# Kernel tuning notes

Hardware: AMD Instinct MI355X
Metric: run time of the kernel (lower is better)

The kernel has to match this reference:

```python
import jax, jax.numpy as jnp
import numpy as np

B, S, HID = 2, 2048, 2048
H, KV, D, E = 16, 4, 128, 32
NB = 9  # num_behavior + 1
EPS = 1e-6
SCALING = (E + D) ** -0.5


def rmsnorm(x, w, eps=EPS):
    # normalize over last dim in fp32, like Qwen3MoeRMSNorm
    xf = x.astype(jnp.float32)
    var = jnp.mean(xf * xf, axis=-1, keepdims=True)
    return (xf * jax.lax.rsqrt(var + eps)).astype(x.dtype) * w


def setup_inputs() -> dict:
    key = jax.random.key(0)
    ks = jax.random.split(key, 12)
    s = lambda n: 1.0 / np.sqrt(n)
    return {
        "hidden_states": jax.random.normal(ks[0], (B, S, HID), jnp.float32),
        "behavior_index": jax.random.randint(ks[1], (B, S), 0, NB),
        "q_proj_w": jax.random.normal(ks[2], (H * D, HID), jnp.float32) * s(HID),
        "k_proj_w": jax.random.normal(ks[3], (KV * D, HID), jnp.float32) * s(HID),
        "v_proj_w": jax.random.normal(ks[4], (KV * D, HID), jnp.float32) * s(HID),
        "o_proj_w": jax.random.normal(ks[5], (HID, H * D), jnp.float32) * s(H * D),
        "q_norm_w": jnp.ones((D,), jnp.float32),
        "k_norm_w": jnp.ones((D,), jnp.float32),
        "qbe_table": jax.random.normal(ks[6], (NB, H * E), jnp.float32),
        "kbe_table": jax.random.normal(ks[7], (NB, KV * E), jnp.float32),
        "qbn_w": jnp.ones((E,), jnp.float32),
        "kbn_w": jnp.ones((E,), jnp.float32),
    }


def reference(hidden_states, behavior_index, q_proj_w, k_proj_w, v_proj_w,
              o_proj_w, q_norm_w, k_norm_w, qbe_table, kbe_table, qbn_w, kbn_w):
    b, s, _ = hidden_states.shape
    # QKV projections + per-head RMSNorm on q/k
    q = rmsnorm((hidden_states @ q_proj_w.T).reshape(b, s, H, D), q_norm_w)
    k = rmsnorm((hidden_states @ k_proj_w.T).reshape(b, s, KV, D), k_norm_w)
    v = (hidden_states @ v_proj_w.T).reshape(b, s, KV, D)
    q = q.transpose(0, 2, 1, 3)  # [b,H,s,D]
    k = k.transpose(0, 2, 1, 3)  # [b,KV,s,D]
    v = v.transpose(0, 2, 1, 3)  # [b,KV,s,D]
    # behavior embeddings: lookup -> per-head RMSNorm -> concat onto head_dim
    qbe = rmsnorm(qbe_table[behavior_index].reshape(b, s, H, E), qbn_w).transpose(0, 2, 1, 3)
    kbe = rmsnorm(kbe_table[behavior_index].reshape(b, s, KV, E), kbn_w).transpose(0, 2, 1, 3)
    q = jnp.concatenate([q, qbe], axis=-1)  # [b,H,s,D+E]
    k = jnp.concatenate([k, kbe], axis=-1)  # [b,KV,s,D+E]
    # GQA: repeat kv heads
    g = H // KV
    k = jnp.repeat(k, g, axis=1)
    v = jnp.repeat(v, g, axis=1)
    # eager attention, causal, softmax in fp32
    scores = jnp.einsum('bhqd,bhkd->bhqk', q, k) * SCALING
    causal = jnp.tril(jnp.ones((s, s), bool))
    scores = jnp.where(causal, scores, jnp.finfo(scores.dtype).min)
    attn = jax.nn.softmax(scores.astype(jnp.float32), axis=-1).astype(q.dtype)
    out = jnp.einsum('bhqk,bhkd->bhqd', attn, v)  # [b,H,s,D]
    out = out.transpose(0, 2, 1, 3).reshape(b, s, H * D)
    return out @ o_proj_w.T
```

## Files before the change

kernel.cpp:

```cpp
#include <hip/hip_runtime.h>

typedef unsigned short u16;
typedef unsigned int u32;
typedef __bf16 bf16x8 __attribute__((ext_vector_type(8)));
typedef __bf16 b16x4 __attribute__((ext_vector_type(4)));
typedef short s16x4 __attribute__((ext_vector_type(4)));
typedef float f32x4 __attribute__((ext_vector_type(4)));

#define SCALE 0.07905694150420949f
#define LOG2E 1.4426950408889634f

__device__ __forceinline__ float bf2f(u16 h) { return __uint_as_float(((u32)h) << 16); }
__device__ __forceinline__ u16 f2bf(float f) {
  u32 u = __float_as_uint(f);
  u += 0x7fffu + ((u >> 16) & 1u);
  return (u16)(u >> 16);
}
__device__ __forceinline__ u16 f2bf_fast(float f) {
  return (u16)((__float_as_uint(f) + 0x8000u) >> 16);
}
__device__ __forceinline__ bf16x8 ldfrag(const u16* p) {
  int4 t = *reinterpret_cast<const int4*>(p);
  return __builtin_bit_cast(bf16x8, t);
}

__device__ __forceinline__ f32x4 mfma16x16(s16x4 a, s16x4 b, f32x4 c) {
#if __has_builtin(__builtin_amdgcn_mfma_f32_16x16x16bf16_1k)
  return __builtin_amdgcn_mfma_f32_16x16x16bf16_1k(a, b, c, 0, 0, 0);
#elif __has_builtin(__builtin_amdgcn_mfma_f32_16x16x16_bf16)
  return __builtin_amdgcn_mfma_f32_16x16x16_bf16(__builtin_bit_cast(b16x4, a),
                                                 __builtin_bit_cast(b16x4, b), c, 0, 0, 0);
#else
  asm volatile("s_nop 2\n\tv_mfma_f32_16x16x16_bf16 %0, %1, %2, %0"
               : "+v"(c) : "v"(a), "v"(b));
  return c;
#endif
}

__device__ __forceinline__ void gld16(const u16* g, u16* l) {
  __builtin_amdgcn_global_load_lds((const __attribute__((address_space(1))) u32*)(const void*)g,
                                   (__attribute__((address_space(3))) u32*)(void*)l, 16, 0, 0);
}

__global__ void conv_all(const float* __restrict__ hs, const float* __restrict__ qw,
                         const float* __restrict__ kw, const float* __restrict__ vw,
                         const float* __restrict__ ow, u16* __restrict__ hs_bf,
                         u16* __restrict__ wqkv, u16* __restrict__ ow_bf) {
  const int total = 4718592;
  for (int i = blockIdx.x * blockDim.x + threadIdx.x; i < total; i += gridDim.x * blockDim.x) {
    const float* src;
    u16* dst;
    int j = i;
    if (j < 2097152) {
      src = hs; dst = hs_bf;
    } else if (j < 3145728) {
      j -= 2097152; src = qw; dst = wqkv;
    } else if (j < 3407872) {
      j -= 3145728; src = kw; dst = wqkv + 4194304;
    } else if (j < 3670016) {
      j -= 3407872; src = vw; dst = wqkv + 5242880;
    } else {
      j -= 3670016; src = ow; dst = ow_bf;
    }
    float4 v = reinterpret_cast<const float4*>(src)[j];
    ushort4 o = {f2bf(v.x), f2bf(v.y), f2bf(v.z), f2bf(v.w)};
    reinterpret_cast<ushort4*>(dst)[j] = o;
  }
}

template <int OUT_BF16>
__global__ __launch_bounds__(256, 2) void gemm_bt(const u16* __restrict__ A,
                                                  const u16* __restrict__ Bw,
                                                  void* __restrict__ Cv,
                                                  int M, int N, int K) {
  __shared__ __align__(16) u16 As[2][8192];
  __shared__ __align__(16) u16 Bs[2][8192];
  const int tid = threadIdx.x;
  const int nbn = N >> 7;
  const int cpx = gridDim.x >> 3;
  const int swz = (blockIdx.x & 7) * cpx + (blockIdx.x >> 3);
  const int bm = swz / nbn, bn = swz % nbn;
  const int row0 = bm << 7, col0 = bn << 7;
  const int lane = tid & 63, w = tid >> 6;
  const int lg = lane >> 4, lr = lane & 15;
  const int wr = w >> 1, wc = w & 1;
  const int nt = K >> 6;

  auto stage = [&](int slot, int t) {
    const size_t k0 = (size_t)t << 6;
#pragma unroll
    for (int it = 0; it < 4; ++it) {
      int G = it * 256 + tid;
      int r = G >> 3, p = G & 7;
      int gs = p ^ (r & 7);
      gld16(&A[(size_t)(row0 + r) * K + k0 + gs * 8], &As[slot][(size_t)G * 8]);
      gld16(&Bw[(size_t)(col0 + r) * K + k0 + gs * 8], &Bs[slot][(size_t)G * 8]);
    }
  };

  f32x4 acc[4][4] = {};
  stage(0, 0);
  if (nt > 1) stage(1, 1);

  for (int t = 0; t < nt; ++t) {
    const int slot = t & 1;
    if (t + 1 < nt) {
      asm volatile("s_waitcnt vmcnt(8)" ::: "memory");
    } else {
      asm volatile("s_waitcnt vmcnt(0)" ::: "memory");
    }
    __builtin_amdgcn_s_barrier();
    __builtin_amdgcn_sched_barrier(0);
#pragma unroll
    for (int kk = 0; kk < 2; ++kk) {
      bf16x8 af[4], bv[4];
#pragma unroll
      for (int m = 0; m < 4; ++m) {
        int r = wr * 64 + m * 16 + lr;
        int g = (kk * 4 + lg) ^ (lr & 7);
        af[m] = ldfrag(&As[slot][r * 64 + g * 8]);
      }
#pragma unroll
      for (int n = 0; n < 4; ++n) {
        int r = wc * 64 + n * 16 + lr;
        int g = (kk * 4 + lg) ^ (lr & 7);
        bv[n] = ldfrag(&Bs[slot][r * 64 + g * 8]);
      }
#pragma unroll
      for (int m = 0; m < 4; ++m)
#pragma unroll
        for (int n = 0; n < 4; ++n)
          acc[m][n] = __builtin_amdgcn_mfma_f32_16x16x32_bf16(af[m], bv[n], acc[m][n], 0, 0, 0);
    }
    __builtin_amdgcn_sched_barrier(0);
    __builtin_amdgcn_s_barrier();
    if (t + 2 < nt) stage(slot, t + 2);
  }

#pragma unroll
  for (int m = 0; m < 4; ++m)
#pragma unroll
    for (int n = 0; n < 4; ++n)
#pragma unroll
      for (int r = 0; r < 4; ++r) {
        int row = row0 + wr * 64 + m * 16 + lg * 4 + r;
        int col = col0 + wc * 64 + n * 16 + lr;
        float v = acc[m][n][r];
        if (OUT_BF16)
          ((u16*)Cv)[(size_t)row * N + col] = f2bf(v);
        else
          ((float*)Cv)[(size_t)row * N + col] = v;
      }
}

__global__ __launch_bounds__(256) void postproc(
    const u16* __restrict__ qkv, const int* __restrict__ bidx,
    const float* __restrict__ qnw, const float* __restrict__ knw,
    const float* __restrict__ qbe_t, const float* __restrict__ kbe_t,
    const float* __restrict__ qbn, const float* __restrict__ kbn,
    u16* __restrict__ qcat, u16* __restrict__ kcat, u16* __restrict__ vt) {
  const int tok = blockIdx.x;
  const int b = tok >> 11, s = tok & 2047;
  const int w = threadIdx.x >> 6, lane = threadIdx.x & 63;
  const int idx = bidx[tok];
  const u16* base = qkv + (size_t)tok * 3072;
  const float QS = SCALE * LOG2E;

  for (int h = w; h < 16; h += 4) {
    float x0 = bf2f(base[h * 128 + 2 * lane]);
    float x1 = bf2f(base[h * 128 + 2 * lane + 1]);
    float ss = x0 * x0 + x1 * x1;
#pragma unroll
    for (int o = 32; o; o >>= 1) ss += __shfl_xor(ss, o);
    float rn = rsqrtf(ss * (1.f / 128.f) + 1e-6f) * QS;
    size_t ob = ((size_t)(b * 16 + h) * 2048 + s) * 160;
    u32 pk = (u32)f2bf(x0 * rn * qnw[2 * lane]) |
             ((u32)f2bf(x1 * rn * qnw[2 * lane + 1]) << 16);
    *reinterpret_cast<u32*>(&qcat[ob + 2 * lane]) = pk;
    if (lane < 32) {
      float e = qbe_t[idx * 512 + h * 32 + lane];
      float s2 = e * e;
#pragma unroll
      for (int o = 16; o; o >>= 1) s2 += __shfl_xor(s2, o);
      qcat[ob + 128 + lane] = f2bf(e * rsqrtf(s2 * (1.f / 32.f) + 1e-6f) * qbn[lane] * QS);
    }
  }
  {
    const int kv = w;
    float x0 = bf2f(base[2048 + kv * 128 + 2 * lane]);
    float x1 = bf2f(base[2048 + kv * 128 + 2 * lane + 1]);
    float ss = x0 * x0 + x1 * x1;
#pragma unroll
    for (int o = 32; o; o >>= 1) ss += __shfl_xor(ss, o);
    float rn = rsqrtf(ss * (1.f / 128.f) + 1e-6f);
    size_t ob = ((size_t)(b * 4 + kv) * 2048 + s) * 160;
    u32 pk = (u32)f2bf(x0 * rn * knw[2 * lane]) |
             ((u32)f2bf(x1 * rn * knw[2 * lane + 1]) << 16);
    *reinterpret_cast<u32*>(&kcat[ob + 2 * lane]) = pk;
    if (lane < 32) {
      float e = kbe_t[idx * 128 + kv * 32 + lane];
      float s2 = e * e;
#pragma unroll
      for (int o = 16; o; o >>= 1) s2 += __shfl_xor(s2, o);
      kcat[ob + 128 + lane] = f2bf(e * rsqrtf(s2 * (1.f / 32.f) + 1e-6f) * kbn[lane]);
    }
    size_t vb = (size_t)(b * 4 + kv) * 128 * 2048;
    vt[vb + (size_t)lane * 2048 + s] = base[2560 + kv * 128 + lane];
    vt[vb + (size_t)(lane + 64) * 2048 + s] = base[2560 + kv * 128 + 64 + lane];
  }
}

__global__ __launch_bounds__(256, 2) void attn(const u16* __restrict__ qcat,
                                               const u16* __restrict__ kcat,
                                               const u16* __restrict__ vt,
                                               u16* __restrict__ aout) {
  __shared__ __align__(16) u16 Kls[2][10240];
  __shared__ __align__(16) u16 Vls[8192];
  const int tid = threadIdx.x;
  const int blk = blockIdx.x;
  const int kvh = blk & 3;
  const int b = (blk >> 2) & 1;
  const int hq = (blk >> 3) & 3;
  const int gsel = blk >> 5;
  const int g = (gsel < 8) ? gsel : 23 - gsel;
  const int h = kvh * 4 + hq;
  const int w = tid >> 6;
  const int lane = tid & 63;
  const int lg = lane >> 4, lr = lane & 15;
  const int qb_a = g * 4 + w;
  const int qb_b = 127 - qb_a;
  const int qpa = qb_a * 16 + lr;
  const int qpb = qb_b * 16 + lr;
  const int nt = 32 - g;

  const u16* qpA = qcat + ((size_t)(b * 16 + h) * 2048 + qb_a * 16) * 160;
  const u16* qpB = qcat + ((size_t)(b * 16 + h) * 2048 + qb_b * 16) * 160;
  bf16x8 qfa[5], qfb[5];
#pragma unroll
  for (int c = 0; c < 5; ++c) {
    qfa[c] = ldfrag(qpA + lr * 160 + c * 32 + lg * 8);
    qfb[c] = ldfrag(qpB + lr * 160 + c * 32 + lg * 8);
  }

  const u16* kbp = kcat + (size_t)(b * 4 + kvh) * 2048 * 160;
  const u16* vbp = vt + (size_t)(b * 4 + kvh) * 128 * 2048;

  auto stageK = [&](int buf, int kt) {
    const u16* ksrc = kbp + (size_t)kt * (64 * 160);
#pragma unroll
    for (int it = 0; it < 5; ++it) {
      int G = it * 256 + tid;
      int r = G / 20, p = G - r * 20;
      int gs = p ^ ((r >> 1) & 3);
      gld16(ksrc + r * 160 + gs * 8, &Kls[buf][G * 8]);
    }
  };
  auto stageV = [&](int kt) {
    const u16* vsrc = vbp + kt * 64;
#pragma unroll
    for (int it = 0; it < 4; ++it) {
      int G = it * 256 + tid;
      int r = G >> 3, p = G & 7;
      int gs = p ^ (r & 7);
      gld16(vsrc + (size_t)r * 2048 + gs * 8, &Vls[G * 8]);
    }
  };

  float ma = -INFINITY, la = 0.f, mb = -INFINITY, lb = 0.f;
  f32x4 acc_a[8] = {}, acc_b[8] = {};

  stageK(0, 0);
  stageV(0);
  __syncthreads();

  for (int kt = 0; kt < nt; ++kt) {
    const int buf = kt & 1;
    const bool aact = (kt <= g);
    if (kt + 1 < nt) stageK(buf ^ 1, kt + 1);

    f32x4 sa[4] = {}, sb[4] = {};
#pragma unroll
    for (int c = 0; c < 5; ++c) {
      bf16x8 kf[4];
#pragma unroll
      for (int i = 0; i < 4; ++i) {
        int r = i * 16 + lr;
        int p = (c * 4 + lg) ^ ((r >> 1) & 3);
        kf[i] = ldfrag(&Kls[buf][(r * 20 + p) * 8]);
      }
#pragma unroll
      for (int i = 0; i < 4; ++i)
        sb[i] = __builtin_amdgcn_mfma_f32_16x16x32_bf16(kf[i], qfb[c], sb[i], 0, 0, 0);
      if (aact)
#pragma unroll
        for (int i = 0; i < 4; ++i)
          sa[i] = __builtin_amdgcn_mfma_f32_16x16x32_bf16(kf[i], qfa[c], sa[i], 0, 0, 0);
    }

    s16x4 pka[4], pkb[4];
    auto soft = [&](f32x4 (&st)[4], float& mm, float& ls, f32x4 (&ac)[8], s16x4 (&pk)[4],
                    bool masked, int qpos) {
      float vmax = -INFINITY;
#pragma unroll
      for (int i = 0; i < 4; ++i)
#pragma unroll
        for (int r = 0; r < 4; ++r) {
          float v = st[i][r];
          if (masked && (kt * 64 + i * 16 + 4 * lg + r > qpos)) v = -INFINITY;
          st[i][r] = v;
          vmax = fmaxf(vmax, v);
        }
      vmax = fmaxf(vmax, __shfl_xor(vmax, 16));
      vmax = fmaxf(vmax, __shfl_xor(vmax, 32));
      bool skip = __all(vmax <= mm + 8.f);
      float mn = skip ? mm : fmaxf(mm, vmax);
      float rs = 0.f;
#pragma unroll
      for (int i = 0; i < 4; ++i)
#pragma unroll
        for (int r = 0; r < 4; ++r) {
          float p = exp2f(st[i][r] - mn);
          st[i][r] = p;
          rs += p;
        }
      rs += __shfl_xor(rs, 16);
      rs += __shfl_xor(rs, 32);
      if (skip) {
        ls += rs;
      } else {
        float corr = exp2f(mm - mn);
        ls = ls * corr + rs;
        mm = mn;
        float c4[4];
#pragma unroll
        for (int r = 0; r < 4; ++r) c4[r] = __shfl(corr, 4 * lg + r);
#pragma unroll
        for (int dt = 0; dt < 8; ++dt)
#pragma unroll
          for (int r = 0; r < 4; ++r) ac[dt][r] *= c4[r];
      }
#pragma unroll
      for (int i = 0; i < 4; ++i) {
        pk[i][0] = (short)f2bf_fast(st[i][0]);
        pk[i][1] = (short)f2bf_fast(st[i][1]);
        pk[i][2] = (short)f2bf_fast(st[i][2]);
        pk[i][3] = (short)f2bf_fast(st[i][3]);
      }
    };
    soft(sb, mb, lb, acc_b, pkb, kt == nt - 1, qpb);
    if (aact) soft(sa, ma, la, acc_a, pka, kt == g, qpa);

    __syncthreads();

#pragma unroll
    for (int ks = 0; ks < 4; ++ks) {
      s16x4 vf[8];
#pragma unroll
      for (int dt = 0; dt < 8; ++dt) {
        int r = dt * 16 + lr;
        int p = (ks * 2 + (lg >> 1)) ^ (r & 7);
        vf[dt] = *reinterpret_cast<const s16x4*>(&Vls[(r * 8 + p) * 8 + (lg & 1) * 4]);
      }
#pragma unroll
      for (int dt = 0; dt < 8; ++dt) acc_b[dt] = mfma16x16(pkb[ks], vf[dt], acc_b[dt]);
      if (aact)
#pragma unroll
        for (int dt = 0; dt < 8; ++dt) acc_a[dt] = mfma16x16(pka[ks], vf[dt], acc_a[dt]);
    }

    __syncthreads();
    if (kt + 1 < nt) stageV(kt + 1);
  }

  float inva[4], invb[4];
#pragma unroll
  for (int r = 0; r < 4; ++r) {
    inva[r] = 1.f / __shfl(la, 4 * lg + r);
    invb[r] = 1.f / __shfl(lb, 4 * lg + r);
  }
#pragma unroll
  for (int dt = 0; dt < 8; ++dt)
#pragma unroll
    for (int r = 0; r < 4; ++r) {
      int rowa = qb_a * 16 + 4 * lg + r;
      int rowb = qb_b * 16 + 4 * lg + r;
      aout[((size_t)(b * 2048 + rowa) * 16 + h) * 128 + dt * 16 + lr] =
          f2bf(acc_a[dt][r] * inva[r]);
      aout[((size_t)(b * 2048 + rowb) * 16 + h) * 128 + dt * 16 + lr] =
          f2bf(acc_b[dt][r] * invb[r]);
    }
}

extern "C" void kernel_launch(void* const* d_in, const int* in_sizes, int n_in,
                              void* d_out, int out_size, void* d_ws, size_t ws_size,
                              hipStream_t stream) {
  const float* hs = (const float*)d_in[0];
  const int* bidx = (const int*)d_in[1];
  const float* qw = (const float*)d_in[2];
  const float* kw = (const float*)d_in[3];
  const float* vw = (const float*)d_in[4];
  const float* ow = (const float*)d_in[5];
  const float* qnw = (const float*)d_in[6];
  const float* knw = (const float*)d_in[7];
  const float* qbe_t = (const float*)d_in[8];
  const float* kbe_t = (const float*)d_in[9];
  const float* qbn = (const float*)d_in[10];
  const float* kbn = (const float*)d_in[11];

  u16* ws = (u16*)d_ws;
  u16* hs_bf = ws;
  u16* wqkv = hs_bf + 8388608;
  u16* ow_bf = wqkv + 6291456;
  u16* qkv = ow_bf + 4194304;
  u16* qcat = qkv + 12582912;
  u16* kcat = qcat + 10485760;
  u16* vt = kcat + 2621440;
  u16* attn_o = vt + 2097152;

  conv_all<<<4608, 256, 0, stream>>>(hs, qw, kw, vw, ow, hs_bf, wqkv, ow_bf);

  gemm_bt<1><<<dim3((4096 / 128) * (3072 / 128)), 256, 0, stream>>>(
      hs_bf, wqkv, (void*)qkv, 4096, 3072, 2048);

  postproc<<<4096, 256, 0, stream>>>(qkv, bidx, qnw, knw, qbe_t, kbe_t, qbn, kbn,
                                     qcat, kcat, vt);

  attn<<<512, 256, 0, stream>>>(qcat, kcat, vt, attn_o);

  gemm_bt<0><<<dim3((4096 / 128) * (2048 / 128)), 256, 0, stream>>>(
      attn_o, ow_bf, (void*)d_out, 4096, 2048, 2048);
}
```

Baseline: 223.1 us.

## Fuse QK RMSNorm, behavior-embedding concat and V transpose into QKV GEMM epilogue

Removes the separate postproc kernel by doing the per-head RMSNorm, behavior-embedding lookup and normalization, and V transpose inside the QKV GEMM epilogue. The sum of squares for each head is reduced across the tile with lane shuffles plus a small shared-memory exchange. This avoids writing and re-reading the bf16 qkv intermediate and saves one launch. In exchange the epilogue writes scalar 2-byte values with scattered strides (especially the V transpose) and adds a barrier and per-thread embedding loops.

Measured after the change: 217.6 us. 2.5% less time.

```diff
diff --git a/kernel.cpp b/kernel.cpp
--- a/kernel.cpp
+++ b/kernel.cpp
@@ -68,13 +68,17 @@
   }
 }
 
-template <int OUT_BF16>
-__global__ __launch_bounds__(256, 2) void gemm_bt(const u16* __restrict__ A,
-                                                  const u16* __restrict__ Bw,
-                                                  void* __restrict__ Cv,
-                                                  int M, int N, int K) {
+template <int MODE>
+__global__ __launch_bounds__(256, 2) void gemm_bt(
+    const u16* __restrict__ A, const u16* __restrict__ Bw, void* __restrict__ Cv,
+    int M, int N, int K,
+    const int* __restrict__ bidx, const float* __restrict__ qnw, const float* __restrict__ knw,
+    const float* __restrict__ qbe_t, const float* __restrict__ kbe_t,
+    const float* __restrict__ qbn, const float* __restrict__ kbn,
+    u16* __restrict__ qcat, u16* __restrict__ kcat, u16* __restrict__ vt) {
   __shared__ __align__(16) u16 As[2][8192];
   __shared__ __align__(16) u16 Bs[2][8192];
+  __shared__ float red[128][2];
   const int tid = threadIdx.x;
   const int nbn = N >> 7;
   const int cpx = gridDim.x >> 3;
@@ -137,76 +141,108 @@
     if (t + 2 < nt) stage(slot, t + 2);
   }
 
-#pragma unroll
-  for (int m = 0; m < 4; ++m)
-#pragma unroll
-    for (int n = 0; n < 4; ++n)
+  if (MODE == 0) {
+#pragma unroll
+    for (int m = 0; m < 4; ++m)
+#pragma unroll
+      for (int n = 0; n < 4; ++n)
+#pragma unroll
+        for (int r = 0; r < 4; ++r) {
+          int row = row0 + wr * 64 + m * 16 + lg * 4 + r;
+          int col = col0 + wc * 64 + n * 16 + lr;
+          ((float*)Cv)[(size_t)row * N + col] = acc[m][n][r];
+        }
+    return;
+  }
+
+  const int cb = col0 >> 7;
+  const float QS = SCALE * LOG2E;
+
+  if (cb < 20) {
+    float part[4][4];
+#pragma unroll
+    for (int m = 0; m < 4; ++m)
 #pragma unroll
       for (int r = 0; r < 4; ++r) {
-        int row = row0 + wr * 64 + m * 16 + lg * 4 + r;
-        int col = col0 + wc * 64 + n * 16 + lr;
-        float v = acc[m][n][r];
-        if (OUT_BF16)
-          ((u16*)Cv)[(size_t)row * N + col] = f2bf(v);
-        else
-          ((float*)Cv)[(size_t)row * N + col] = v;
-      }
-}
-
-__global__ __launch_bounds__(256) void postproc(
-    const u16* __restrict__ qkv, const int* __restrict__ bidx,
-    const float* __restrict__ qnw, const float* __restrict__ knw,
-    const float* __restrict__ qbe_t, const float* __restrict__ kbe_t,
-    const float* __restrict__ qbn, const float* __restrict__ kbn,
-    u16* __restrict__ qcat, u16* __restrict__ kcat, u16* __restrict__ vt) {
-  const int tok = blockIdx.x;
-  const int b = tok >> 11, s = tok & 2047;
-  const int w = threadIdx.x >> 6, lane = threadIdx.x & 63;
-  const int idx = bidx[tok];
-  const u16* base = qkv + (size_t)tok * 3072;
-  const float QS = SCALE * LOG2E;
-
-  for (int h = w; h < 16; h += 4) {
-    float x0 = bf2f(base[h * 128 + 2 * lane]);
-    float x1 = bf2f(base[h * 128 + 2 * lane + 1]);
-    float ss = x0 * x0 + x1 * x1;
-#pragma unroll
-    for (int o = 32; o; o >>= 1) ss += __shfl_xor(ss, o);
-    float rn = rsqrtf(ss * (1.f / 128.f) + 1e-6f) * QS;
-    size_t ob = ((size_t)(b * 16 + h) * 2048 + s) * 160;
-    u32 pk = (u32)f2bf(x0 * rn * qnw[2 * lane]) |
-             ((u32)f2bf(x1 * rn * qnw[2 * lane + 1]) << 16);
-    *reinterpret_cast<u32*>(&qcat[ob + 2 * lane]) = pk;
-    if (lane < 32) {
-      float e = qbe_t[idx * 512 + h * 32 + lane];
-      float s2 = e * e;
-#pragma unroll
-      for (int o = 16; o; o >>= 1) s2 += __shfl_xor(s2, o);
-      qcat[ob + 128 + lane] = f2bf(e * rsqrtf(s2 * (1.f / 32.f) + 1e-6f) * qbn[lane] * QS);
-    }
-  }
-  {
-    const int kv = w;
-    float x0 = bf2f(base[2048 + kv * 128 + 2 * lane]);
-    float x1 = bf2f(base[2048 + kv * 128 + 2 * lane + 1]);
-    float ss = x0 * x0 + x1 * x1;
-#pragma unroll
-    for (int o = 32; o; o >>= 1) ss += __shfl_xor(ss, o);
-    float rn = rsqrtf(ss * (1.f / 128.f) + 1e-6f);
-    size_t ob = ((size_t)(b * 4 + kv) * 2048 + s) * 160;
-    u32 pk = (u32)f2bf(x0 * rn * knw[2 * lane]) |
-             ((u32)f2bf(x1 * rn * knw[2 * lane + 1]) << 16);
-    *reinterpret_cast<u32*>(&kcat[ob + 2 * lane]) = pk;
-    if (lane < 32) {
-      float e = kbe_t[idx * 128 + kv * 32 + lane];
-      float s2 = e * e;
-#pragma unroll
-      for (int o = 16; o; o >>= 1) s2 += __shfl_xor(s2, o);
-      kcat[ob + 128 + lane] = f2bf(e * rsqrtf(s2 * (1.f / 32.f) + 1e-6f) * kbn[lane]);
-    }
-    size_t vb = (size_t)(b * 4 + kv) * 128 * 2048;
-    vt[vb + (size_t)lane * 2048 + s] = base[2560 + kv * 128 + lane];
-    vt[vb + (size_t)(lane + 64) * 2048 + s] = base[2560 + kv * 128 + 64 + lane];
+        float s = 0.f;
+#pragma unroll
+        for (int n = 0; n < 4; ++n) s += acc[m][n][r] * acc[m][n][r];
+#pragma unroll
+        for (int o = 1; o < 16; o <<= 1) s += __shfl_xor(s, o);
+        part[m][r] = s;
+      }
+    if (lr == 0) {
+#pragma unroll
+      for (int m = 0; m < 4; ++m)
+#pragma unroll
+        for (int r = 0; r < 4; ++r) red[wr * 64 + m * 16 + lg * 4 + r][wc] = part[m][r];
+    }
+    __syncthreads();
+
+    const bool isq = (cb < 16);
+    const float* nw = isq ? qnw : knw;
+    u16* outp = isq ? qcat : kcat;
+    const int hb = isq ? (16 * 2048) : (4 * 2048);
+    const int hh = isq ? cb : (cb - 16);
+#pragma unroll
+    for (int m = 0; m < 4; ++m)
+#pragma unroll
+      for (int r = 0; r < 4; ++r) {
+        int rl = wr * 64 + m * 16 + lg * 4 + r;
+        float ss = red[rl][0] + red[rl][1];
+        float rn = rsqrtf(ss * (1.f / 128.f) + 1e-6f) * (isq ? QS : 1.f);
+        int token = row0 + rl;
+        int bb = token >> 11, s = token & 2047;
+        size_t ob = ((size_t)(bb * hb) + (size_t)hh * 2048 + s) * 160;
+#pragma unroll
+        for (int n = 0; n < 4; ++n) {
+          int d = wc * 64 + n * 16 + lr;
+          outp[ob + d] = f2bf(acc[m][n][r] * rn * nw[d]);
+        }
+      }
+    if (tid < 128) {
+      int token = row0 + tid;
+      int bb = token >> 11, s = token & 2047;
+      int idx = bidx[token];
+      const float* ep;
+      const float* bw;
+      float qs;
+      size_t ob;
+      if (isq) {
+        ep = qbe_t + idx * 512 + hh * 32;
+        bw = qbn;
+        qs = QS;
+        ob = ((size_t)(bb * 16 + hh) * 2048 + s) * 160 + 128;
+      } else {
+        ep = kbe_t + idx * 128 + hh * 32;
+        bw = kbn;
+        qs = 1.f;
+        ob = ((size_t)(bb * 4 + hh) * 2048 + s) * 160 + 128;
+      }
+      float ss = 0.f;
+#pragma unroll
+      for (int e = 0; e < 32; ++e) {
+        float v = ep[e];
+        ss += v * v;
+      }
+      float rn = rsqrtf(ss * (1.f / 32.f) + 1e-6f) * qs;
+#pragma unroll
+      for (int e = 0; e < 32; ++e) outp[ob + e] = f2bf(ep[e] * rn * bw[e]);
+    }
+  } else {
+    const int kv = cb - 20;
+#pragma unroll
+    for (int m = 0; m < 4; ++m)
+#pragma unroll
+      for (int r = 0; r < 4; ++r) {
+        int token = row0 + wr * 64 + m * 16 + lg * 4 + r;
+        int bb = token >> 11, s = token & 2047;
+#pragma unroll
+        for (int n = 0; n < 4; ++n) {
+          int d = wc * 64 + n * 16 + lr;
+          vt[((size_t)(bb * 4 + kv) * 128 + d) * 2048 + s] = f2bf(acc[m][n][r]);
+        }
+      }
   }
 }
 
@@ -419,14 +455,14 @@
 
   conv_all<<<4608, 256, 0, stream>>>(hs, qw, kw, vw, ow, hs_bf, wqkv, ow_bf);
 
-  gemm_bt<1><<<dim3((4096 / 128) * (3072 / 128)), 256, 0, stream>>>(
-      hs_bf, wqkv, (void*)qkv, 4096, 3072, 2048);
-
-  postproc<<<4096, 256, 0, stream>>>(qkv, bidx, qnw, knw, qbe_t, kbe_t, qbn, kbn,
-                                     qcat, kcat, vt);
+  gemm_bt<2><<<dim3((4096 / 128) * (3072 / 128)), 256, 0, stream>>>(
+      hs_bf, wqkv, nullptr, 4096, 3072, 2048,
+      bidx, qnw, knw, qbe_t, kbe_t, qbn, kbn, qcat, kcat, vt);
 
   attn<<<512, 256, 0, stream>>>(qcat, kcat, vt, attn_o);
 
   gemm_bt<0><<<dim3((4096 / 128) * (2048 / 128)), 256, 0, stream>>>(
-      attn_o, ow_bf, (void*)d_out, 4096, 2048, 2048);
-}
+      attn_o, ow_bf, (void*)d_out, 4096, 2048, 2048,
+      nullptr, nullptr, nullptr, nullptr, nullptr, nullptr, nullptr,
+      nullptr, nullptr, nullptr);
+}
```
